# Kernel tuning notes

Measured on AMD Instinct MI355X. Metric: run time of the kernel, lower is better.

Reference implementation:

```python
import jax, jax.numpy as jnp
import numpy as np

K = 9
SIGMA = 4.0
RADIUS = 16  # round(4*sigma)
IMAGE_SHAPE = (256, 256)


def _gaussian_kernel_1d():
    i = jnp.arange(2 * RADIUS + 1, dtype=jnp.float32) - RADIUS
    g = jnp.exp(-(i ** 2) / (2.0 * SIGMA ** 2))
    return g / jnp.sum(g)


def _gaussian_blur(x):
    # x: [b, H, W, 1]; separable Gaussian blur, reflect-101 borders (cv2 default)
    g = _gaussian_kernel_1d()
    xp = jnp.pad(x, ((0, 0), (RADIUS, RADIUS), (RADIUS, RADIUS), (0, 0)), mode='reflect')
    dn = ('NHWC', 'HWIO', 'NHWC')
    kv = g.reshape(2 * RADIUS + 1, 1, 1, 1)  # vertical pass
    kh = g.reshape(1, 2 * RADIUS + 1, 1, 1)  # horizontal pass
    y = jax.lax.conv_general_dilated(xp, kv, (1, 1), 'VALID', dimension_numbers=dn)
    y = jax.lax.conv_general_dilated(y, kh, (1, 1), 'VALID', dimension_numbers=dn)
    return y


def setup_inputs() -> dict:
    key = jax.random.key(0)
    k1, k2 = jax.random.split(key)
    inputs = jax.random.normal(k1, (8, 32, 32, 512), dtype=jnp.float32)
    feature_vector = jax.random.normal(k2, (16384, 512), dtype=jnp.float32)
    return {"inputs": inputs, "feature_vector": feature_vector}


def reference(inputs, feature_vector):
    b, h, w, c = inputs.shape
    feat = inputs.reshape(b * h * w, c)
    # pairwise euclidean distances: [b*h*w, N]
    d2 = (jnp.sum(feat ** 2, axis=-1, keepdims=True)
          + jnp.sum(feature_vector ** 2, axis=-1)[None, :]
          - 2.0 * feat @ feature_vector.T)
    dist = jnp.sqrt(jnp.maximum(d2, 0.0))
    # k smallest distances, ascending (equivalent to tf.sort(...)[..., :k])
    neg_topk, _ = jax.lax.top_k(-dist, K)
    score = -neg_topk  # [b*h*w, K], ascending
    mask = score[:, 0].reshape(b, h, w, 1)
    score = score.reshape(b, h * w, K)
    # patch with maximal nearest-neighbor distance
    idx = jnp.argmax(score[..., 0], axis=-1)  # [b]
    conf = jnp.take_along_axis(score, idx[:, None, None], axis=1)[:, 0, :]  # [b, K]
    exp_conf = jnp.exp(conf)
    weight = 1.0 - jnp.max(exp_conf, axis=-1) / jnp.sum(exp_conf, axis=-1)
    score_out = (jnp.max(score[..., 0], axis=-1) * weight)[:, None]  # [b, 1]
    mask = jax.image.resize(mask, (b, *IMAGE_SHAPE, 1), method='bilinear', antialias=False)
    mask = _gaussian_blur(mask)
    return score_out, mask
```

## Files before the change

### kernel.cpp

```cpp
#include <hip/hip_runtime.h>

typedef __attribute__((ext_vector_type(8))) short bf16x8;
typedef __attribute__((ext_vector_type(4))) float f32x4;

static constexpr int M = 8192;
static constexpr int N = 16384;
static constexpr int K = 512;
static constexpr int BM = 128;
static constexpr int BN = 128;
static constexpr int BK = 64;
static constexpr int KCHUNKS = K / BK;
static constexpr int NGROUPS_S = 8;
static constexpr int GROUP_N_S = N / NGROUPS_S;
static constexpr int NTILES_S = GROUP_N_S / BN;
static constexpr int NGROUPS_F = 16;
static constexpr int GROUP_N_F = N / NGROUPS_F;
static constexpr int NTILES_F = GROUP_N_F / BN;
static constexpr int NCHUNK = NTILES_F * KCHUNKS;
static constexpr float F_INF = 3.0e38f;

__device__ __forceinline__ unsigned short f2bf(float f) {
    unsigned int u = __float_as_uint(f);
    return (unsigned short)((u + 0x7fffu + ((u >> 16) & 1u)) >> 16);
}

__device__ __forceinline__ void gl_lds16(const unsigned short* g, unsigned short* l) {
    __builtin_amdgcn_global_load_lds(
        (const __attribute__((address_space(1))) unsigned int*)g,
        (__attribute__((address_space(3))) unsigned int*)l, 16, 0, 0);
}

__global__ void k_prep(const float* __restrict__ Q, const float* __restrict__ F,
                       unsigned short* __restrict__ Qb, unsigned short* __restrict__ Fb,
                       float* __restrict__ qn, float* __restrict__ fn) {
    int wid = blockIdx.x * 4 + (threadIdx.x >> 6);
    int lane = threadIdx.x & 63;
    bool isQ = wid < M;
    const float* src = isQ ? (Q + (size_t)wid * K) : (F + (size_t)(wid - M) * K);
    unsigned short* dst = isQ ? (Qb + (size_t)wid * K) : (Fb + (size_t)(wid - M) * K);
    const float4* p = reinterpret_cast<const float4*>(src) + lane * 2;
    float4 a = p[0], b = p[1];
    float s = a.x*a.x + a.y*a.y + a.z*a.z + a.w*a.w
            + b.x*b.x + b.y*b.y + b.z*b.z + b.w*b.w;
    bf16x8 v;
    v[0]=(short)f2bf(a.x); v[1]=(short)f2bf(a.y); v[2]=(short)f2bf(a.z); v[3]=(short)f2bf(a.w);
    v[4]=(short)f2bf(b.x); v[5]=(short)f2bf(b.y); v[6]=(short)f2bf(b.z); v[7]=(short)f2bf(b.w);
    *reinterpret_cast<bf16x8*>(dst + lane * 8) = v;
    #pragma unroll
    for (int d = 1; d < 64; d <<= 1) s += __shfl_xor(s, d);
    if (lane == 0) { if (isQ) qn[wid] = s; else fn[wid - M] = s; }
}

__global__ void k_norms(const float* __restrict__ Q, const float* __restrict__ F,
                        float* __restrict__ qn, float* __restrict__ fn) {
    int wid = blockIdx.x * 4 + (threadIdx.x >> 6);
    int lane = threadIdx.x & 63;
    const float* src = (wid < M) ? (Q + (size_t)wid * K) : (F + (size_t)(wid - M) * K);
    const float4* p = reinterpret_cast<const float4*>(src) + lane * 2;
    float4 a = p[0], b = p[1];
    float s = a.x*a.x + a.y*a.y + a.z*a.z + a.w*a.w
            + b.x*b.x + b.y*b.y + b.z*b.z + b.w*b.w;
    #pragma unroll
    for (int d = 1; d < 64; d <<= 1) s += __shfl_xor(s, d);
    if (lane == 0) { if (wid < M) qn[wid] = s; else fn[wid - M] = s; }
}

__global__ __launch_bounds__(256, 2)
void k_mingemm2(const unsigned short* __restrict__ Qb, const unsigned short* __restrict__ Fb,
                const float* __restrict__ qn, const float* __restrict__ fn,
                float* __restrict__ pv, unsigned int* __restrict__ pi) {
    __shared__ unsigned short As[2][BM * BK];
    __shared__ unsigned short Bs[2][BN * BK];
    __shared__ float qn_t[BM];
    __shared__ float fn_g[GROUP_N_F];

    const int tid = threadIdx.x;
    const int lane = tid & 63;
    const int wave = tid >> 6;
    const int wr = wave >> 1, wc = wave & 1;
    const int l15 = lane & 15, l4 = lane >> 4;

    const int wg = blockIdx.x;
    const int swz = (wg & 7) * 128 + (wg >> 3);
    const int group = swz >> 6;
    const int rowblk = swz & 63;
    const int row0 = rowblk * BM;
    const int gbase = group * GROUP_N_F;

    const int r_l = lane >> 3, p8 = lane & 7;
    const int g8 = p8 ^ r_l;
    const unsigned short* gA[4];
    const unsigned short* gB[4];
    #pragma unroll
    for (int i = 0; i < 4; ++i) {
        int row = (wave * 4 + i) * 8 + r_l;
        gA[i] = Qb + (size_t)(row0 + row) * K + g8 * 8;
        gB[i] = Fb + (size_t)(gbase + row) * K + g8 * 8;
    }

    auto stage = [&](int ct, int buf) {
        const int kc = ct & 7;
        const size_t bo = (size_t)(ct >> 3) * BN * K;
        #pragma unroll
        for (int i = 0; i < 4; ++i) gl_lds16(gA[i] + kc * BK, &As[buf][(wave * 4 + i) * 512]);
        #pragma unroll
        for (int i = 0; i < 4; ++i) gl_lds16(gB[i] + bo + kc * BK, &Bs[buf][(wave * 4 + i) * 512]);
    };

    for (int i = tid; i < GROUP_N_F; i += 256) fn_g[i] = fn[gbase + i];
    if (tid < BM) qn_t[tid] = qn[row0 + tid];
    stage(0, 0);
    __syncthreads();

    float qnv[4][4];
    #pragma unroll
    for (int fi = 0; fi < 4; ++fi)
        #pragma unroll
        for (int j = 0; j < 4; ++j)
            qnv[fi][j] = qn_t[wr*64 + fi*16 + l4*4 + j];

    float mval[4][4];
    unsigned int midx[4][4];
    #pragma unroll
    for (int a = 0; a < 4; ++a)
        #pragma unroll
        for (int b = 0; b < 4; ++b) { mval[a][b] = F_INF; midx[a][b] = 0; }

    int cur = 0;
    for (int nt = 0; nt < NTILES_F; ++nt) {
        f32x4 acc[4][4];
        #pragma unroll
        for (int a = 0; a < 4; ++a)
            #pragma unroll
            for (int b = 0; b < 4; ++b) acc[a][b] = f32x4{0.f, 0.f, 0.f, 0.f};

        for (int kc = 0; kc < KCHUNKS; ++kc) {
            const int ct = nt * KCHUNKS + kc;
            if (ct + 1 < NCHUNK) {
                stage(ct + 1, cur ^ 1);
                asm volatile("s_waitcnt vmcnt(8)" ::: "memory");
            } else {
                asm volatile("s_waitcnt vmcnt(0)" ::: "memory");
            }
            __builtin_amdgcn_sched_barrier(0);
            __builtin_amdgcn_s_barrier();
            #pragma unroll
            for (int ks = 0; ks < 2; ++ks) {
                const int gidx = ks * 4 + l4;
                bf16x8 af[4], bfv[4];
                #pragma unroll
                for (int fi = 0; fi < 4; ++fi) {
                    int r = wr*64 + fi*16 + l15;
                    int pg = gidx ^ (r & 7);
                    af[fi] = *reinterpret_cast<const bf16x8*>(&As[cur][r*BK + pg*8]);
                }
                #pragma unroll
                for (int fj = 0; fj < 4; ++fj) {
                    int r = wc*64 + fj*16 + l15;
                    int pg = gidx ^ (r & 7);
                    bfv[fj] = *reinterpret_cast<const bf16x8*>(&Bs[cur][r*BK + pg*8]);
                }
                #pragma unroll
                for (int fi = 0; fi < 4; ++fi)
                    #pragma unroll
                    for (int fj = 0; fj < 4; ++fj)
                        acc[fi][fj] = __builtin_amdgcn_mfma_f32_16x16x32_bf16(
                            af[fi], bfv[fj], acc[fi][fj], 0, 0, 0);
            }
            __builtin_amdgcn_sched_barrier(0);
            __builtin_amdgcn_s_barrier();
            cur ^= 1;
        }
        const int colb = gbase + nt * BN + wc * 64;
        float fnv[4];
        #pragma unroll
        for (int fj = 0; fj < 4; ++fj) fnv[fj] = fn_g[nt*BN + wc*64 + fj*16 + l15];
        #pragma unroll
        for (int fi = 0; fi < 4; ++fi) {
            #pragma unroll
            for (int j = 0; j < 4; ++j) {
                float qv = qnv[fi][j];
                #pragma unroll
                for (int fj = 0; fj < 4; ++fj) {
                    float d2 = qv + fnv[fj] - 2.0f * acc[fi][fj][j];
                    if (d2 < mval[fi][j]) {
                        mval[fi][j] = d2;
                        midx[fi][j] = (unsigned int)(colb + fj*16 + l15);
                    }
                }
            }
        }
    }
    #pragma unroll
    for (int fi = 0; fi < 4; ++fi) {
        #pragma unroll
        for (int j = 0; j < 4; ++j) {
            float v = mval[fi][j];
            unsigned int ix = midx[fi][j];
            #pragma unroll
            for (int d = 1; d < 16; d <<= 1) {
                float ov = __shfl_xor(v, d);
                unsigned int oi = (unsigned int)__shfl_xor((int)ix, d);
                if (ov < v) { v = ov; ix = oi; }
            }
            if (l15 == 0) {
                int rg = row0 + wr*64 + fi*16 + l4*4 + j;
                int pidx = rg * 32 + group*2 + wc;
                pv[pidx] = v;
                pi[pidx] = ix;
            }
        }
    }
}

__global__ __launch_bounds__(256, 2)
void k_mingemm_cast(const float* __restrict__ Q, const float* __restrict__ F,
                    const float* __restrict__ qn, const float* __restrict__ fn,
                    float* __restrict__ pv, unsigned int* __restrict__ pi) {
    __shared__ unsigned short As[BM * BK];
    __shared__ unsigned short Bs[BN * BK];
    __shared__ float qn_t[BM];
    __shared__ float fn_t[BN];

    const int tid = threadIdx.x;
    const int lane = tid & 63;
    const int wave = tid >> 6;
    const int wr = wave >> 1, wc = wave & 1;
    const int l15 = lane & 15, l4 = lane >> 4;

    const int row0 = blockIdx.x * BM;
    const int gbase = blockIdx.y * GROUP_N_S;

    const int srow = tid >> 3;
    const int p8 = tid & 7;
    const int g8 = p8 ^ (srow & 7);
    const float* pA[4];
    const float* pB[4];
    int dstOff[4];
    #pragma unroll
    for (int i = 0; i < 4; ++i) {
        int r = i * 32 + srow;
        pA[i] = Q + (size_t)(row0 + r) * K + g8 * 8;
        pB[i] = F + (size_t)(gbase + r) * K + g8 * 8;
        dstOff[i] = r * BK + p8 * 8;
    }

    float mval[4][4];
    unsigned int midx[4][4];
    float qnv[4][4];
    #pragma unroll
    for (int a = 0; a < 4; ++a)
        #pragma unroll
        for (int b = 0; b < 4; ++b) { mval[a][b] = F_INF; midx[a][b] = 0; qnv[a][b] = 0.f; }

    for (int nt = 0; nt < NTILES_S; ++nt) {
        f32x4 acc[4][4];
        #pragma unroll
        for (int a = 0; a < 4; ++a)
            #pragma unroll
            for (int b = 0; b < 4; ++b) acc[a][b] = f32x4{0.f, 0.f, 0.f, 0.f};

        for (int kc = 0; kc < KCHUNKS; ++kc) {
            __syncthreads();
            #pragma unroll
            for (int i = 0; i < 4; ++i) {
                const float4* sa = reinterpret_cast<const float4*>(pA[i] + kc * BK);
                float4 xa = sa[0], ya = sa[1];
                const float4* sb = reinterpret_cast<const float4*>(pB[i] + nt * (BN * K) + kc * BK);
                float4 xb = sb[0], yb = sb[1];
                bf16x8 va, vb;
                va[0]=(short)f2bf(xa.x); va[1]=(short)f2bf(xa.y); va[2]=(short)f2bf(xa.z); va[3]=(short)f2bf(xa.w);
                va[4]=(short)f2bf(ya.x); va[5]=(short)f2bf(ya.y); va[6]=(short)f2bf(ya.z); va[7]=(short)f2bf(ya.w);
                vb[0]=(short)f2bf(xb.x); vb[1]=(short)f2bf(xb.y); vb[2]=(short)f2bf(xb.z); vb[3]=(short)f2bf(xb.w);
                vb[4]=(short)f2bf(yb.x); vb[5]=(short)f2bf(yb.y); vb[6]=(short)f2bf(yb.z); vb[7]=(short)f2bf(yb.w);
                *reinterpret_cast<bf16x8*>(&As[dstOff[i]]) = va;
                *reinterpret_cast<bf16x8*>(&Bs[dstOff[i]]) = vb;
            }
            if (kc == 0) {
                if (nt == 0 && tid < BM) qn_t[tid] = qn[row0 + tid];
                if (tid < BN) fn_t[tid] = fn[gbase + nt * BN + tid];
            }
            __syncthreads();
            if (nt == 0 && kc == 0) {
                #pragma unroll
                for (int fi = 0; fi < 4; ++fi)
                    #pragma unroll
                    for (int j = 0; j < 4; ++j)
                        qnv[fi][j] = qn_t[wr*64 + fi*16 + l4*4 + j];
            }
            #pragma unroll
            for (int ks = 0; ks < 2; ++ks) {
                const int gidx = ks * 4 + l4;
                bf16x8 af[4], bfv[4];
                #pragma unroll
                for (int fi = 0; fi < 4; ++fi) {
                    int r = wr*64 + fi*16 + l15;
                    int pg = gidx ^ (r & 7);
                    af[fi] = *reinterpret_cast<const bf16x8*>(&As[r*BK + pg*8]);
                }
                #pragma unroll
                for (int fj = 0; fj < 4; ++fj) {
                    int r = wc*64 + fj*16 + l15;
                    int pg = gidx ^ (r & 7);
                    bfv[fj] = *reinterpret_cast<const bf16x8*>(&Bs[r*BK + pg*8]);
                }
                #pragma unroll
                for (int fi = 0; fi < 4; ++fi)
                    #pragma unroll
                    for (int fj = 0; fj < 4; ++fj)
                        acc[fi][fj] = __builtin_amdgcn_mfma_f32_16x16x32_bf16(
                            af[fi], bfv[fj], acc[fi][fj], 0, 0, 0);
            }
        }
        const int colb = gbase + nt * BN + wc * 64;
        float fnv[4];
        #pragma unroll
        for (int fj = 0; fj < 4; ++fj) fnv[fj] = fn_t[wc*64 + fj*16 + l15];
        #pragma unroll
        for (int fi = 0; fi < 4; ++fi) {
            #pragma unroll
            for (int j = 0; j < 4; ++j) {
                float qv = qnv[fi][j];
                #pragma unroll
                for (int fj = 0; fj < 4; ++fj) {
                    float d2 = qv + fnv[fj] - 2.0f * acc[fi][fj][j];
                    if (d2 < mval[fi][j]) {
                        mval[fi][j] = d2;
                        midx[fi][j] = (unsigned int)(colb + fj*16 + l15);
                    }
                }
            }
        }
    }
    #pragma unroll
    for (int fi = 0; fi < 4; ++fi) {
        #pragma unroll
        for (int j = 0; j < 4; ++j) {
            float v = mval[fi][j];
            unsigned int ix = midx[fi][j];
            #pragma unroll
            for (int d = 1; d < 16; d <<= 1) {
                float ov = __shfl_xor(v, d);
                unsigned int oi = (unsigned int)__shfl_xor((int)ix, d);
                if (ov < v) { v = ov; ix = oi; }
            }
            if (l15 == 0) {
                int rg = row0 + wr*64 + fi*16 + l4*4 + j;
                int pidx = rg * 16 + blockIdx.y * 2 + wc;
                pv[pidx] = v;
                pi[pidx] = ix;
            }
        }
    }
}

__global__ void k_refine(const float* __restrict__ Q, const float* __restrict__ F,
                         const float* __restrict__ pv, const unsigned int* __restrict__ pi,
                         float* __restrict__ minD, int PS) {
    int row = blockIdx.x * 4 + (threadIdx.x >> 6);
    int lane = threadIdx.x & 63;
    float v = F_INF; unsigned int ix = 0;
    if (lane < PS) { v = pv[row*PS + lane]; ix = pi[row*PS + lane]; }
    #pragma unroll
    for (int d = 1; d < 64; d <<= 1) {
        float ov = __shfl_xor(v, d);
        unsigned int oi = (unsigned int)__shfl_xor((int)ix, d);
        if (ov < v) { v = ov; ix = oi; }
    }
    const float4* q = reinterpret_cast<const float4*>(Q + (size_t)row * K) + lane*2;
    const float4* f = reinterpret_cast<const float4*>(F + (size_t)ix * K) + lane*2;
    float4 a0 = q[0], a1 = q[1], b0 = f[0], b1 = f[1];
    float s = 0.f, dx;
    dx = a0.x-b0.x; s += dx*dx;  dx = a0.y-b0.y; s += dx*dx;
    dx = a0.z-b0.z; s += dx*dx;  dx = a0.w-b0.w; s += dx*dx;
    dx = a1.x-b1.x; s += dx*dx;  dx = a1.y-b1.y; s += dx*dx;
    dx = a1.z-b1.z; s += dx*dx;  dx = a1.w-b1.w; s += dx*dx;
    #pragma unroll
    for (int d = 1; d < 64; d <<= 1) s += __shfl_xor(s, d);
    if (lane == 0) minD[row] = sqrtf(s);
}

__global__ void k_argmax(const float* __restrict__ minD, unsigned int* __restrict__ sel) {
    __shared__ float sv[256];
    __shared__ int si[256];
    int b = blockIdx.x, tid = threadIdx.x;
    float bv = -F_INF; int bi = 0;
    for (int p = tid; p < 1024; p += 256) {
        float v = minD[b*1024 + p];
        if (v > bv) { bv = v; bi = p; }
    }
    sv[tid] = bv; si[tid] = bi;
    __syncthreads();
    for (int s = 128; s > 0; s >>= 1) {
        if (tid < s) {
            if (sv[tid+s] > sv[tid] || (sv[tid+s] == sv[tid] && si[tid+s] < si[tid])) {
                sv[tid] = sv[tid+s]; si[tid] = si[tid+s];
            }
        }
        __syncthreads();
    }
    if (tid == 0) sel[b] = (unsigned int)(b*1024 + si[0]);
}

__global__ void k_dist8(const float* __restrict__ Q, const float* __restrict__ F,
                        const unsigned int* __restrict__ sel, float* __restrict__ d2all) {
    __shared__ float qs[8][512];
    int tid = threadIdx.x;
    int lane = tid & 63, wave = tid >> 6;
    for (int i = tid; i < 8*512; i += 256) {
        int b = i >> 9;
        qs[b][i & 511] = Q[(size_t)sel[b] * K + (i & 511)];
    }
    __syncthreads();
    int base = blockIdx.x * 128 + wave * 32;
    for (int r = 0; r < 32; ++r) {
        int row = base + r;
        const float4* fp = reinterpret_cast<const float4*>(F + (size_t)row * K) + lane*2;
        float4 f0 = fp[0], f1 = fp[1];
        float fv[8] = {f0.x,f0.y,f0.z,f0.w,f1.x,f1.y,f1.z,f1.w};
        float accb[8];
        #pragma unroll
        for (int b = 0; b < 8; ++b) {
            float s = 0.f;
            #pragma unroll
            for (int e = 0; e < 8; ++e) {
                float d = fv[e] - qs[b][lane*8 + e];
                s += d * d;
            }
            accb[b] = s;
        }
        #pragma unroll
        for (int d = 1; d < 64; d <<= 1)
            #pragma unroll
            for (int b = 0; b < 8; ++b) accb[b] += __shfl_xor(accb[b], d);
        if (lane == 0) {
            #pragma unroll
            for (int b = 0; b < 8; ++b) d2all[b * N + row] = accb[b];
        }
    }
}

__global__ void k_sel9(const float* __restrict__ d2all, float* __restrict__ out) {
    __shared__ float sv[256 * 10];
    int b = blockIdx.x, tid = threadIdx.x;
    float v[9];
    #pragma unroll
    for (int i = 0; i < 9; ++i) v[i] = F_INF;
    for (int i = tid; i < N; i += 256) {
        float x = d2all[b * N + i];
        #pragma unroll
        for (int s = 0; s < 9; ++s) {
            float lo = fminf(v[s], x), hi = fmaxf(v[s], x);
            v[s] = lo; x = hi;
        }
    }
    #pragma unroll
    for (int i = 0; i < 9; ++i) sv[tid*10 + i] = v[i];
    sv[tid*10 + 9] = F_INF;
    __syncthreads();
    for (int s = 128; s > 0; s >>= 1) {
        if (tid < s) {
            int ia = 1, ib = 1;
            float av = sv[tid*10], bv = sv[(tid+s)*10];
            float c[9];
            #pragma unroll
            for (int k = 0; k < 9; ++k) {
                bool ta = av <= bv;
                c[k] = ta ? av : bv;
                float na = sv[tid*10 + ia], nb = sv[(tid+s)*10 + ib];
                if (ta) { av = na; ++ia; } else { bv = nb; ++ib; }
            }
            #pragma unroll
            for (int k = 0; k < 9; ++k) sv[tid*10 + k] = c[k];
        }
        __syncthreads();
    }
    if (tid == 0) {
        float c[9];
        #pragma unroll
        for (int i = 0; i < 9; ++i) c[i] = sqrtf(fmaxf(sv[i], 0.f));
        float S = 0.f;
        #pragma unroll
        for (int i = 0; i < 9; ++i) S += expf(c[i] - c[8]);
        out[b] = c[0] * (1.f - 1.f / S);
    }
}

__global__ void k_top9(const float* __restrict__ Q, const float* __restrict__ F,
                       const unsigned int* __restrict__ sel, float* __restrict__ part9) {
    __shared__ float qs[512];
    __shared__ float dist[2048];
    __shared__ float rv[256];
    __shared__ int ri[256];
    int b = blockIdx.x >> 3, g = blockIdx.x & 7;
    int tid = threadIdx.x;
    unsigned int srow = sel[b];
    if (tid < 128)
        reinterpret_cast<float4*>(qs)[tid] =
            reinterpret_cast<const float4*>(Q + (size_t)srow * K)[tid];
    __syncthreads();
    #pragma unroll
    for (int e = 0; e < 8; ++e) {
        int fl = tid + 256*e;
        const float* fp = F + (size_t)(g*2048 + fl) * K;
        float s = 0.f;
        for (int k = 0; k < 512; k += 4) {
            float4 fv4 = *reinterpret_cast<const float4*>(fp + k);
            float d0 = qs[k]   - fv4.x;
            float d1 = qs[k+1] - fv4.y;
            float d2 = qs[k+2] - fv4.z;
            float d3 = qs[k+3] - fv4.w;
            s += d0*d0 + d1*d1 + d2*d2 + d3*d3;
        }
        dist[fl] = s;
    }
    __syncthreads();
    for (int it = 0; it < 9; ++it) {
        float lv = F_INF; int li = 0;
        #pragma unroll
        for (int e = 0; e < 8; ++e) {
            int idx = tid + 256*e;
            float v = dist[idx];
            if (v < lv) { lv = v; li = idx; }
        }
        rv[tid] = lv; ri[tid] = li;
        __syncthreads();
        for (int s = 128; s > 0; s >>= 1) {
            if (tid < s && rv[tid+s] < rv[tid]) { rv[tid] = rv[tid+s]; ri[tid] = ri[tid+s]; }
            __syncthreads();
        }
        if (tid == 0) {
            part9[(b*8+g)*9 + it] = rv[0];
            dist[ri[0]] = F_INF;
        }
        __syncthreads();
    }
}

__global__ void k_final(const float* __restrict__ part9, float* __restrict__ out) {
    int b = threadIdx.x;
    if (b >= 8) return;
    float arr[9];
    #pragma unroll
    for (int i = 0; i < 9; ++i) arr[i] = F_INF;
    for (int g = 0; g < 8; ++g)
        for (int i = 0; i < 9; ++i) {
            float v = part9[(b*8+g)*9 + i];
            #pragma unroll
            for (int s = 0; s < 9; ++s) {
                float lo = fminf(arr[s], v), hi = fmaxf(arr[s], v);
                arr[s] = lo; v = hi;
            }
        }
    float c[9];
    #pragma unroll
    for (int i = 0; i < 9; ++i) c[i] = sqrtf(fmaxf(arr[i], 0.f));
    float c8 = c[8], S = 0.f;
    #pragma unroll
    for (int i = 0; i < 9; ++i) S += expf(c[i] - c8);
    float w = 1.f - 1.f / S;
    out[b] = c[0] * w;
}

__global__ void k_wmat(float* __restrict__ W) {
    int idx = blockIdx.x * 256 + threadIdx.x;
    int o = idx >> 5, j = idx & 31;
    float gsum = 0.f;
    #pragma unroll
    for (int u = 0; u < 33; ++u) { float d = (float)(u - 16); gsum += expf(-d*d * (1.f/32.f)); }
    float acc = 0.f;
    for (int u = 0; u < 33; ++u) {
        float d = (float)(u - 16);
        float gu = expf(-d*d * (1.f/32.f));
        int y = o + u - 16;
        y = y < 0 ? -y : (y > 255 ? 510 - y : y);
        float xin = ((float)y + 0.5f) * 0.125f - 0.5f;
        float j0f = floorf(xin);
        int j0 = (int)j0f;
        float wfr = xin - j0f;
        float r;
        if (j0 < 0) r = (j == 0) ? 1.f : 0.f;
        else if (j0 >= 31) r = (j == 31) ? 1.f : 0.f;
        else r = (j == j0) ? (1.f - wfr) : ((j == j0 + 1) ? wfr : 0.f);
        acc += gu * r;
    }
    W[idx] = acc / gsum;
}

__global__ void k_mask(const float* __restrict__ minD, const float* __restrict__ W,
                       float* __restrict__ outm) {
    __shared__ float Ms[1024];
    __shared__ float Ws[8192];
    __shared__ float Ts[8192];
    int b = blockIdx.x, tid = threadIdx.x;
    for (int i = tid; i < 1024; i += 256) Ms[i] = minD[b*1024 + i];
    for (int i = tid; i < 8192; i += 256) Ws[i] = W[i];
    __syncthreads();
    {
        int o = tid;
        float wrow[32];
        #pragma unroll
        for (int i = 0; i < 32; ++i) wrow[i] = Ws[o*32 + i];
        for (int j = 0; j < 32; ++j) {
            float s = 0.f;
            #pragma unroll
            for (int i = 0; i < 32; ++i) s += wrow[i] * Ms[i*32 + j];
            Ts[o*32 + j] = s;
        }
    }
    __syncthreads();
    {
        int p = tid;
        float wp[32];
        #pragma unroll
        for (int j = 0; j < 32; ++j) wp[j] = Ws[p*32 + j];
        float* dst = outm + (size_t)b * 65536;
        for (int o = 0; o < 256; ++o) {
            float s = 0.f;
            #pragma unroll
            for (int j = 0; j < 32; ++j) s += Ts[o*32 + j] * wp[j];
            dst[o*256 + p] = s;
        }
    }
}

extern "C" void kernel_launch(void* const* d_in, const int* in_sizes, int n_in,
                              void* d_out, int out_size, void* d_ws, size_t ws_size,
                              hipStream_t stream) {
    const float* Q = (const float*)d_in[0];
    const float* F = (const float*)d_in[1];
    float* out = (float*)d_out;

    const size_t smallFloats = (size_t)8192*32*2 + 8192 + 8 + 576 + (size_t)8*N + 8192 + 16384 + 8192;
    const size_t REQ = smallFloats*4 + (size_t)M*K*2 + (size_t)N*K*2;
    const bool fast = ws_size >= REQ;
    const int PS = fast ? 32 : 16;

    float* ws = (float*)d_ws;
    float* pv = ws;
    unsigned int* pi = (unsigned int*)(pv + 8192*PS);
    float* minD = (float*)(pi + 8192*PS);
    unsigned int* sel = (unsigned int*)(minD + 8192);
    float* part9 = (float*)(sel + 8);
    float* d2all = part9 + 576;
    float* qn = d2all + (size_t)8*N;
    float* fn = qn + 8192;
    float* W  = fn + 16384;
    unsigned short* Qb = (unsigned short*)(W + 8192);
    unsigned short* Fb = Qb + (size_t)M*K;

    k_wmat <<<dim3(32), 256, 0, stream>>>(W);
    if (fast) {
        k_prep <<<dim3((M + N) / 4), 256, 0, stream>>>(Q, F, Qb, Fb, qn, fn);
        k_mingemm2<<<dim3(M / BM * NGROUPS_F), 256, 0, stream>>>(Qb, Fb, qn, fn, pv, pi);
        k_refine<<<dim3(M / 4), 256, 0, stream>>>(Q, F, pv, pi, minD, PS);
        k_argmax<<<dim3(8), 256, 0, stream>>>(minD, sel);
        k_dist8<<<dim3(N / 128), 256, 0, stream>>>(Q, F, sel, d2all);
        k_sel9 <<<dim3(8), 256, 0, stream>>>(d2all, out);
    } else {
        k_norms<<<dim3((M + N) / 4), 256, 0, stream>>>(Q, F, qn, fn);
        k_mingemm_cast<<<dim3(M / BM, NGROUPS_S), 256, 0, stream>>>(Q, F, qn, fn, pv, pi);
        k_refine<<<dim3(M / 4), 256, 0, stream>>>(Q, F, pv, pi, minD, PS);
        k_argmax<<<dim3(8), 256, 0, stream>>>(minD, sel);
        k_top9 <<<dim3(64), 256, 0, stream>>>(Q, F, sel, part9);
        k_final<<<dim3(1), 64, 0, stream>>>(part9, out);
    }
    k_mask <<<dim3(8), 256, 0, stream>>>(minD, W, out + 8);
}
```

Baseline: 346.4 us.

## Switch nearest-neighbor GEMM to FP8 MFMA with top-6 exact refinement

Input and feature rows are now quantized to FP8 e4m3 in a pre-swizzled layout, and the min-distance GEMM uses fp8 MFMA instructions. This halves operand bytes and raises peak matrix throughput. Because FP8 is less precise, the refine kernel takes the 6 best approximate candidates per row and recomputes their exact fp32 distances instead of just the single best. The change also adds an occupancy hint of 4, s_setprio around the MFMA block, and a new block swizzle, at the risk of missing the true nearest neighbor when FP8 error is large.

```diff
diff --git a/kernel.cpp b/kernel.cpp
--- a/kernel.cpp
+++ b/kernel.cpp
@@ -10,13 +10,16 @@
 static constexpr int BN = 128;
 static constexpr int BK = 64;
 static constexpr int KCHUNKS = K / BK;
-static constexpr int NGROUPS_S = 8;
-static constexpr int GROUP_N_S = N / NGROUPS_S;
-static constexpr int NTILES_S = GROUP_N_S / BN;
 static constexpr int NGROUPS_F = 16;
 static constexpr int GROUP_N_F = N / NGROUPS_F;
 static constexpr int NTILES_F = GROUP_N_F / BN;
 static constexpr int NCHUNK = NTILES_F * KCHUNKS;
+static constexpr int BMs = 128;
+static constexpr int BKs = 64;
+static constexpr int KCHUNKS_S = K / BKs;
+static constexpr int NGROUPS_S = 8;
+static constexpr int GROUP_N_S = N / NGROUPS_S;
+static constexpr int NTILES_S = GROUP_N_S / 128;
 static constexpr float F_INF = 3.0e38f;
 
 __device__ __forceinline__ unsigned short f2bf(float f) {
@@ -24,31 +27,67 @@
     return (unsigned short)((u + 0x7fffu + ((u >> 16) & 1u)) >> 16);
 }
 
-__device__ __forceinline__ void gl_lds16(const unsigned short* g, unsigned short* l) {
+__device__ __forceinline__ unsigned int f2e4m3(float f) {
+    unsigned int u = __float_as_uint(f);
+    unsigned int sign = (u >> 24) & 0x80u;
+    unsigned int au = u & 0x7fffffffu;
+    if (au == 0) return sign;
+    int e = (int)(au >> 23) - 127;
+    unsigned int m = (au & 0x7fffffu) | 0x800000u;
+    int ef = e + 7;
+    if (ef > 15) return sign | 0x7e;
+    int sh = (ef < 1) ? (21 - ef) : 20;
+    if (sh > 30) return sign;
+    unsigned int keep = m >> sh;
+    unsigned int rem = m & ((1u << sh) - 1u);
+    unsigned int half = 1u << (sh - 1);
+    keep += (rem > half) || (rem == half && (keep & 1u));
+    unsigned int enc = (ef < 1) ? keep : ((unsigned int)(ef << 3) + keep - 8u);
+    if (enc >= 0x7fu) enc = 0x7eu;
+    return sign | enc;
+}
+
+template <bool HI>
+__device__ __forceinline__ unsigned int cvt2_fp8(float x, float y, unsigned int old) {
+#if __has_builtin(__builtin_amdgcn_cvt_pk_fp8_f32)
+    return (unsigned int)__builtin_amdgcn_cvt_pk_fp8_f32(x, y, (int)old, HI);
+#else
+    unsigned int v = f2e4m3(x) | (f2e4m3(y) << 8);
+    return HI ? ((old & 0x0000ffffu) | (v << 16)) : ((old & 0xffff0000u) | v);
+#endif
+}
+
+__device__ __forceinline__ void gl_lds16(const void* g, void* l) {
     __builtin_amdgcn_global_load_lds(
         (const __attribute__((address_space(1))) unsigned int*)g,
         (__attribute__((address_space(3))) unsigned int*)l, 16, 0, 0);
 }
 
-__global__ void k_prep(const float* __restrict__ Q, const float* __restrict__ F,
-                       unsigned short* __restrict__ Qb, unsigned short* __restrict__ Fb,
-                       float* __restrict__ qn, float* __restrict__ fn) {
+__global__ void k_prep8(const float* __restrict__ Q, const float* __restrict__ F,
+                        unsigned char* __restrict__ Q8, unsigned char* __restrict__ F8,
+                        float* __restrict__ qn, float* __restrict__ fn) {
     int wid = blockIdx.x * 4 + (threadIdx.x >> 6);
     int lane = threadIdx.x & 63;
     bool isQ = wid < M;
-    const float* src = isQ ? (Q + (size_t)wid * K) : (F + (size_t)(wid - M) * K);
-    unsigned short* dst = isQ ? (Qb + (size_t)wid * K) : (Fb + (size_t)(wid - M) * K);
+    int r = isQ ? wid : wid - M;
+    const float* src = isQ ? (Q + (size_t)wid * K) : (F + (size_t)r * K);
+    unsigned char* dst = (isQ ? Q8 : F8) + (size_t)r * K;
     const float4* p = reinterpret_cast<const float4*>(src) + lane * 2;
     float4 a = p[0], b = p[1];
     float s = a.x*a.x + a.y*a.y + a.z*a.z + a.w*a.w
             + b.x*b.x + b.y*b.y + b.z*b.z + b.w*b.w;
-    bf16x8 v;
-    v[0]=(short)f2bf(a.x); v[1]=(short)f2bf(a.y); v[2]=(short)f2bf(a.z); v[3]=(short)f2bf(a.w);
-    v[4]=(short)f2bf(b.x); v[5]=(short)f2bf(b.y); v[6]=(short)f2bf(b.z); v[7]=(short)f2bf(b.w);
-    *reinterpret_cast<bf16x8*>(dst + lane * 8) = v;
+    unsigned int lo = 0, hi = 0;
+    lo = cvt2_fp8<false>(a.x, a.y, lo);
+    lo = cvt2_fp8<true >(a.z, a.w, lo);
+    hi = cvt2_fp8<false>(b.x, b.y, hi);
+    hi = cvt2_fp8<true >(b.z, b.w, hi);
+    int g = lane & 7, kc = lane >> 3;
+    int off = kc * 64 + (((g >> 1) ^ (r & 3)) << 4) + (((g & 1) ^ ((r >> 2) & 1)) << 3);
+    uint2 v2; v2.x = lo; v2.y = hi;
+    *reinterpret_cast<uint2*>(dst + off) = v2;
     #pragma unroll
     for (int d = 1; d < 64; d <<= 1) s += __shfl_xor(s, d);
-    if (lane == 0) { if (isQ) qn[wid] = s; else fn[wid - M] = s; }
+    if (lane == 0) { if (isQ) qn[wid] = s; else fn[r] = s; }
 }
 
 __global__ void k_norms(const float* __restrict__ Q, const float* __restrict__ F,
@@ -65,12 +104,12 @@
     if (lane == 0) { if (wid < M) qn[wid] = s; else fn[wid - M] = s; }
 }
 
-__global__ __launch_bounds__(256, 2)
-void k_mingemm2(const unsigned short* __restrict__ Qb, const unsigned short* __restrict__ Fb,
+__global__ __launch_bounds__(256, 4)
+void k_mingemm6(const unsigned char* __restrict__ Q8, const unsigned char* __restrict__ F8,
                 const float* __restrict__ qn, const float* __restrict__ fn,
                 float* __restrict__ pv, unsigned int* __restrict__ pi) {
-    __shared__ unsigned short As[2][BM * BK];
-    __shared__ unsigned short Bs[2][BN * BK];
+    __shared__ unsigned char As[2][BM * BK];
+    __shared__ unsigned char Bs[2][BN * BK];
     __shared__ float qn_t[BM];
     __shared__ float fn_g[GROUP_N_F];
 
@@ -81,30 +120,28 @@
     const int l15 = lane & 15, l4 = lane >> 4;
 
     const int wg = blockIdx.x;
-    const int swz = (wg & 7) * 128 + (wg >> 3);
-    const int group = swz >> 6;
-    const int rowblk = swz & 63;
-    const int row0 = rowblk * BM;
+    const int x = wg & 7, q = wg >> 3;
+    const int group = x * 2 + (q & 1);
+    const int rblk = q >> 1;
+    const int row0 = rblk * BM;
     const int gbase = group * GROUP_N_F;
 
-    const int r_l = lane >> 3, p8 = lane & 7;
-    const int g8 = p8 ^ r_l;
-    const unsigned short* gA[4];
-    const unsigned short* gB[4];
-    #pragma unroll
-    for (int i = 0; i < 4; ++i) {
-        int row = (wave * 4 + i) * 8 + r_l;
-        gA[i] = Qb + (size_t)(row0 + row) * K + g8 * 8;
-        gB[i] = Fb + (size_t)(gbase + row) * K + g8 * 8;
+    const unsigned char* gA[2];
+    const unsigned char* gB[2];
+    #pragma unroll
+    for (int i = 0; i < 2; ++i) {
+        int rowl = (wave * 2 + i) * 16 + (lane >> 2);
+        gA[i] = Q8 + (size_t)(row0 + rowl) * K + (lane & 3) * 16;
+        gB[i] = F8 + (size_t)(gbase + rowl) * K + (lane & 3) * 16;
     }
 
     auto stage = [&](int ct, int buf) {
         const int kc = ct & 7;
         const size_t bo = (size_t)(ct >> 3) * BN * K;
         #pragma unroll
-        for (int i = 0; i < 4; ++i) gl_lds16(gA[i] + kc * BK, &As[buf][(wave * 4 + i) * 512]);
-        #pragma unroll
-        for (int i = 0; i < 4; ++i) gl_lds16(gB[i] + bo + kc * BK, &Bs[buf][(wave * 4 + i) * 512]);
+        for (int i = 0; i < 2; ++i) gl_lds16(gA[i] + kc * BK, &As[buf][(wave*2 + i) * 1024]);
+        #pragma unroll
+        for (int i = 0; i < 2; ++i) gl_lds16(gB[i] + bo + kc * BK, &Bs[buf][(wave*2 + i) * 1024]);
     };
 
     for (int i = tid; i < GROUP_N_F; i += 256) fn_g[i] = fn[gbase + i];
@@ -138,7 +175,7 @@
             const int ct = nt * KCHUNKS + kc;
             if (ct + 1 < NCHUNK) {
                 stage(ct + 1, cur ^ 1);
-                asm volatile("s_waitcnt vmcnt(8)" ::: "memory");
+                asm volatile("s_waitcnt vmcnt(4)" ::: "memory");
             } else {
                 asm volatile("s_waitcnt vmcnt(0)" ::: "memory");
             }
@@ -146,26 +183,29 @@
             __builtin_amdgcn_s_barrier();
             #pragma unroll
             for (int ks = 0; ks < 2; ++ks) {
-                const int gidx = ks * 4 + l4;
-                bf16x8 af[4], bfv[4];
+                long long af[4], bfv[4];
                 #pragma unroll
                 for (int fi = 0; fi < 4; ++fi) {
                     int r = wr*64 + fi*16 + l15;
-                    int pg = gidx ^ (r & 7);
-                    af[fi] = *reinterpret_cast<const bf16x8*>(&As[cur][r*BK + pg*8]);
+                    int g = ks*4 + l4;
+                    int off = r*BK + (((g >> 1) ^ (r & 3)) << 4) + (((g & 1) ^ ((r >> 2) & 1)) << 3);
+                    af[fi] = *reinterpret_cast<const long long*>(&As[cur][off]);
                 }
                 #pragma unroll
                 for (int fj = 0; fj < 4; ++fj) {
                     int r = wc*64 + fj*16 + l15;
-                    int pg = gidx ^ (r & 7);
-                    bfv[fj] = *reinterpret_cast<const bf16x8*>(&Bs[cur][r*BK + pg*8]);
+                    int g = ks*4 + l4;
+                    int off = r*BK + (((g >> 1) ^ (r & 3)) << 4) + (((g & 1) ^ ((r >> 2) & 1)) << 3);
+                    bfv[fj] = *reinterpret_cast<const long long*>(&Bs[cur][off]);
                 }
+                __builtin_amdgcn_s_setprio(1);
                 #pragma unroll
                 for (int fi = 0; fi < 4; ++fi)
                     #pragma unroll
                     for (int fj = 0; fj < 4; ++fj)
-                        acc[fi][fj] = __builtin_amdgcn_mfma_f32_16x16x32_bf16(
+                        acc[fi][fj] = __builtin_amdgcn_mfma_f32_16x16x32_fp8_fp8(
                             af[fi], bfv[fj], acc[fi][fj], 0, 0, 0);
+                __builtin_amdgcn_s_setprio(0);
             }
             __builtin_amdgcn_sched_barrier(0);
             __builtin_amdgcn_s_barrier();
@@ -217,10 +257,10 @@
 void k_mingemm_cast(const float* __restrict__ Q, const float* __restrict__ F,
                     const float* __restrict__ qn, const float* __restrict__ fn,
                     float* __restrict__ pv, unsigned int* __restrict__ pi) {
-    __shared__ unsigned short As[BM * BK];
-    __shared__ unsigned short Bs[BN * BK];
-    __shared__ float qn_t[BM];
-    __shared__ float fn_t[BN];
+    __shared__ unsigned short As[BMs * BKs];
+    __shared__ unsigned short Bs[BMs * BKs];
+    __shared__ float qn_t[BMs];
+    __shared__ float fn_t[BMs];
 
     const int tid = threadIdx.x;
     const int lane = tid & 63;
@@ -228,7 +268,7 @@
     const int wr = wave >> 1, wc = wave & 1;
     const int l15 = lane & 15, l4 = lane >> 4;
 
-    const int row0 = blockIdx.x * BM;
+    const int row0 = blockIdx.x * BMs;
     const int gbase = blockIdx.y * GROUP_N_S;
 
     const int srow = tid >> 3;
@@ -242,7 +282,7 @@
         int r = i * 32 + srow;
         pA[i] = Q + (size_t)(row0 + r) * K + g8 * 8;
         pB[i] = F + (size_t)(gbase + r) * K + g8 * 8;
-        dstOff[i] = r * BK + p8 * 8;
+        dstOff[i] = r * BKs + p8 * 8;
     }
 
     float mval[4][4];
@@ -260,13 +300,13 @@
             #pragma unroll
             for (int b = 0; b < 4; ++b) acc[a][b] = f32x4{0.f, 0.f, 0.f, 0.f};
 
-        for (int kc = 0; kc < KCHUNKS; ++kc) {
+        for (int kc = 0; kc < KCHUNKS_S; ++kc) {
             __syncthreads();
             #pragma unroll
             for (int i = 0; i < 4; ++i) {
-                const float4* sa = reinterpret_cast<const float4*>(pA[i] + kc * BK);
+                const float4* sa = reinterpret_cast<const float4*>(pA[i] + kc * BKs);
                 float4 xa = sa[0], ya = sa[1];
-                const float4* sb = reinterpret_cast<const float4*>(pB[i] + nt * (BN * K) + kc * BK);
+                const float4* sb = reinterpret_cast<const float4*>(pB[i] + nt * (128 * K) + kc * BKs);
                 float4 xb = sb[0], yb = sb[1];
                 bf16x8 va, vb;
                 va[0]=(short)f2bf(xa.x); va[1]=(short)f2bf(xa.y); va[2]=(short)f2bf(xa.z); va[3]=(short)f2bf(xa.w);
@@ -277,8 +317,8 @@
                 *reinterpret_cast<bf16x8*>(&Bs[dstOff[i]]) = vb;
             }
             if (kc == 0) {
-                if (nt == 0 && tid < BM) qn_t[tid] = qn[row0 + tid];
-                if (tid < BN) fn_t[tid] = fn[gbase + nt * BN + tid];
+                if (nt == 0 && tid < BMs) qn_t[tid] = qn[row0 + tid];
+                if (tid < 128) fn_t[tid] = fn[gbase + nt * 128 + tid];
             }
             __syncthreads();
             if (nt == 0 && kc == 0) {
@@ -296,13 +336,13 @@
                 for (int fi = 0; fi < 4; ++fi) {
                     int r = wr*64 + fi*16 + l15;
                     int pg = gidx ^ (r & 7);
-                    af[fi] = *reinterpret_cast<const bf16x8*>(&As[r*BK + pg*8]);
+                    af[fi] = *reinterpret_cast<const bf16x8*>(&As[r*BKs + pg*8]);
                 }
                 #pragma unroll
                 for (int fj = 0; fj < 4; ++fj) {
                     int r = wc*64 + fj*16 + l15;
                     int pg = gidx ^ (r & 7);
-                    bfv[fj] = *reinterpret_cast<const bf16x8*>(&Bs[r*BK + pg*8]);
+                    bfv[fj] = *reinterpret_cast<const bf16x8*>(&Bs[r*BKs + pg*8]);
                 }
                 #pragma unroll
                 for (int fi = 0; fi < 4; ++fi)
@@ -312,7 +352,7 @@
                             af[fi], bfv[fj], acc[fi][fj], 0, 0, 0);
             }
         }
-        const int colb = gbase + nt * BN + wc * 64;
+        const int colb = gbase + nt * 128 + wc * 64;
         float fnv[4];
         #pragma unroll
         for (int fj = 0; fj < 4; ++fj) fnv[fj] = fn_t[wc*64 + fj*16 + l15];
@@ -354,13 +394,56 @@
     }
 }
 
+__global__ void k_refine2(const float* __restrict__ Q, const float* __restrict__ F,
+                          const float* __restrict__ pv, const unsigned int* __restrict__ pi,
+                          float* __restrict__ minD) {
+    int row = blockIdx.x * 4 + (threadIdx.x >> 6);
+    int lane = threadIdx.x & 63;
+    float v = F_INF; unsigned int ix = 0;
+    if (lane < 32) { v = pv[(size_t)row*32 + lane]; ix = pi[(size_t)row*32 + lane]; }
+    unsigned int cand[6];
+    #pragma unroll
+    for (int c = 0; c < 6; ++c) {
+        float bv = v; unsigned int bix = ix; int bl = lane;
+        #pragma unroll
+        for (int d = 1; d < 64; d <<= 1) {
+            float ov = __shfl_xor(bv, d);
+            unsigned int oix = (unsigned int)__shfl_xor((int)bix, d);
+            int obl = __shfl_xor(bl, d);
+            if (ov < bv || (ov == bv && obl < bl)) { bv = ov; bix = oix; bl = obl; }
+        }
+        cand[c] = bix;
+        if (lane == bl) v = F_INF;
+    }
+    const float4* qp = reinterpret_cast<const float4*>(Q + (size_t)row * K) + lane*2;
+    float4 a0 = qp[0], a1 = qp[1];
+    float best = F_INF;
+    #pragma unroll
+    for (int c = 0; c < 6; ++c) {
+        const float4* fp = reinterpret_cast<const float4*>(F + (size_t)cand[c] * K) + lane*2;
+        float4 b0 = fp[0], b1 = fp[1];
+        float s = 0.f, dx;
+        dx = a0.x-b0.x; s += dx*dx;  dx = a0.y-b0.y; s += dx*dx;
+        dx = a0.z-b0.z; s += dx*dx;  dx = a0.w-b0.w; s += dx*dx;
+        dx = a1.x-b1.x; s += dx*dx;  dx = a1.y-b1.y; s += dx*dx;
+        dx = a1.z-b1.z; s += dx*dx;  dx = a1.w-b1.w; s += dx*dx;
+        #pragma unroll
+        for (int d = 1; d < 64; d <<= 1) s += __shfl_xor(s, d);
+        best = fminf(best, s);
+    }
+    if (lane == 0) minD[row] = sqrtf(best);
+}
+
 __global__ void k_refine(const float* __restrict__ Q, const float* __restrict__ F,
                          const float* __restrict__ pv, const unsigned int* __restrict__ pi,
                          float* __restrict__ minD, int PS) {
     int row = blockIdx.x * 4 + (threadIdx.x >> 6);
     int lane = threadIdx.x & 63;
     float v = F_INF; unsigned int ix = 0;
-    if (lane < PS) { v = pv[row*PS + lane]; ix = pi[row*PS + lane]; }
+    for (int t = lane; t < PS; t += 64) {
+        float nv = pv[(size_t)row*PS + t];
+        if (nv < v) { v = nv; ix = pi[(size_t)row*PS + t]; }
+    }
     #pragma unroll
     for (int d = 1; d < 64; d <<= 1) {
         float ov = __shfl_xor(v, d);
@@ -631,36 +714,35 @@
     const float* F = (const float*)d_in[1];
     float* out = (float*)d_out;
 
-    const size_t smallFloats = (size_t)8192*32*2 + 8192 + 8 + 576 + (size_t)8*N + 8192 + 16384 + 8192;
+    const size_t smallFloats = (size_t)8192*64*2 + 8192 + 8 + 576 + (size_t)8*N + 8192 + 16384 + 8192;
     const size_t REQ = smallFloats*4 + (size_t)M*K*2 + (size_t)N*K*2;
     const bool fast = ws_size >= REQ;
-    const int PS = fast ? 32 : 16;
 
     float* ws = (float*)d_ws;
     float* pv = ws;
-    unsigned int* pi = (unsigned int*)(pv + 8192*PS);
-    float* minD = (float*)(pi + 8192*PS);
+    unsigned int* pi = (unsigned int*)(pv + 8192*64);
+    float* minD = (float*)(pi + 8192*64);
     unsigned int* sel = (unsigned int*)(minD + 8192);
     float* part9 = (float*)(sel + 8);
     float* d2all = part9 + 576;
     float* qn = d2all + (size_t)8*N;
     float* fn = qn + 8192;
     float* W  = fn + 16384;
-    unsigned short* Qb = (unsigned short*)(W + 8192);
-    unsigned short* Fb = Qb + (size_t)M*K;
+    unsigned char* Q8 = (unsigned char*)(W + 8192);
+    unsigned char* F8 = Q8 + (size_t)M*K;
 
     k_wmat <<<dim3(32), 256, 0, stream>>>(W);
     if (fast) {
-        k_prep <<<dim3((M + N) / 4), 256, 0, stream>>>(Q, F, Qb, Fb, qn, fn);
-        k_mingemm2<<<dim3(M / BM * NGROUPS_F), 256, 0, stream>>>(Qb, Fb, qn, fn, pv, pi);
-        k_refine<<<dim3(M / 4), 256, 0, stream>>>(Q, F, pv, pi, minD, PS);
+        k_prep8<<<dim3((M + N) / 4), 256, 0, stream>>>(Q, F, Q8, F8, qn, fn);
+        k_mingemm6<<<dim3(64 * NGROUPS_F), 256, 0, stream>>>(Q8, F8, qn, fn, pv, pi);
+        k_refine2<<<dim3(M / 4), 256, 0, stream>>>(Q, F, pv, pi, minD);
         k_argmax<<<dim3(8), 256, 0, stream>>>(minD, sel);
         k_dist8<<<dim3(N / 128), 256, 0, stream>>>(Q, F, sel, d2all);
         k_sel9 <<<dim3(8), 256, 0, stream>>>(d2all, out);
     } else {
         k_norms<<<dim3((M + N) / 4), 256, 0, stream>>>(Q, F, qn, fn);
-        k_mingemm_cast<<<dim3(M / BM, NGROUPS_S), 256, 0, stream>>>(Q, F, qn, fn, pv, pi);
-        k_refine<<<dim3(M / 4), 256, 0, stream>>>(Q, F, pv, pi, minD, PS);
+        k_mingemm_cast<<<dim3(M / BMs, NGROUPS_S), 256, 0, stream>>>(Q, F, qn, fn, pv, pi);
+        k_refine<<<dim3(M / 4), 256, 0, stream>>>(Q, F, pv, pi, minD, 16);
         k_argmax<<<dim3(8), 256, 0, stream>>>(minD, sel);
         k_top9 <<<dim3(64), 256, 0, stream>>>(Q, F, sel, part9);
         k_final<<<dim3(1), 64, 0, stream>>>(part9, out);
```

After: 376.2 us. 1.09x slower.
